# Kernel optimization log

Measured on AMD Instinct MI355X. Metric: run time of the kernel, lower is better.

Reference implementation:

```python
import jax, jax.numpy as jnp
import numpy as np

WINDOW_SIZE = 11
SIGMA = 1.5
K2 = 0.03
PAD = WINDOW_SIZE // 2


def _gaussian_window(size, sigma):
    coords = np.arange(size, dtype=np.float32) - size // 2
    g = np.exp(-coords ** 2 / (2.0 * sigma ** 2))
    g = g / g.sum()
    w2d = np.outer(g, g)  # [size, size]
    return jnp.asarray(w2d[None, None], dtype=jnp.float32)  # [1,1,size,size]


def _blur(x, w):
    # x: [B,1,H,W], w: [1,1,k,k]; SAME zero padding, matches F.conv2d(padding=k//2)
    return jax.lax.conv_general_dilated(
        x, w, window_strides=(1, 1), padding=[(PAD, PAD), (PAD, PAD)],
        dimension_numbers=("NCHW", "OIHW", "NCHW"))


def setup_inputs() -> dict:
    key = jax.random.key(0)
    k1, k2 = jax.random.split(key)
    B, C, H, W = 32, 1, 512, 512
    inp = jax.random.uniform(k1, (B, C, H, W), dtype=jnp.float32)
    tgt = jax.random.uniform(k2, (B, C, H, W), dtype=jnp.float32)
    mask = jnp.ones((B, C, H, W), dtype=jnp.float32)
    window = _gaussian_window(WINDOW_SIZE, SIGMA)
    return {"input": inp, "target": tgt, "mask": mask, "window": window}


def reference(input, target, mask, window):
    # mask application (mask path is always exercised, matching the torch code)
    inp = input * mask
    tgt = target * mask

    mw = _blur(mask, window) + 1e-08  # blurred mask normalizer

    mu_i = _blur(inp, window) / mw
    mu_t = _blur(tgt, window) / mw

    sigma_i_sq = _blur(inp * inp, window) / mw - mu_i * mu_i
    sigma_t_sq = _blur(tgt * tgt, window) / mw - mu_t * mu_t
    sigma_it = _blur(inp * tgt, window) / mw - mu_i * mu_t

    L = jnp.maximum(jnp.max(inp), jnp.max(tgt))
    C2 = (K2 * L) ** 2
    C3 = C2 / 2.0

    sigma_i = jnp.sqrt(jax.nn.relu(sigma_i_sq) + 1e-12)
    sigma_t = jnp.sqrt(jax.nn.relu(sigma_t_sq) + 1e-12)

    structure_map = (sigma_it + C3) / (sigma_i * sigma_t + C3 + 1e-08)
    return 1.0 - jnp.mean(structure_map)
```

## Files before the change

kernel.cpp:

```cpp
#include <hip/hip_runtime.h>
#include <math.h>

#define BATCH 32
#define H 512
#define W 512
#define TX 32
#define TY 32
#define SX 44
#define NPIX (32LL*512*512)

__device__ inline void atomicMaxFloat(float* addr, float val) {
    unsigned int* ua = (unsigned int*)addr;
    unsigned int old = __float_as_uint(*addr);
    while (true) {
        float of = __uint_as_float(old);
        if (of >= val) break;
        unsigned int assumed = old;
        old = atomicCAS(ua, assumed, __float_as_uint(val));
        if (old == assumed) break;
    }
}

__global__ void init_kernel(double* sum, float* mx) {
    *sum = 0.0;
    *mx = -INFINITY;
}

__global__ __launch_bounds__(256) void maxred_kernel(
        const float* __restrict__ in, const float* __restrict__ tg,
        const float* __restrict__ mk, float* mx) {
    const float4* in4 = (const float4*)in;
    const float4* tg4 = (const float4*)tg;
    const float4* mk4 = (const float4*)mk;
    long long n4 = NPIX / 4;
    long long idx = (long long)blockIdx.x * blockDim.x + threadIdx.x;
    long long stride = (long long)gridDim.x * blockDim.x;
    float m = -INFINITY;
    for (long long i = idx; i < n4; i += stride) {
        float4 a = in4[i], b = tg4[i], c = mk4[i];
        m = fmaxf(m, fmaxf(a.x * c.x, b.x * c.x));
        m = fmaxf(m, fmaxf(a.y * c.y, b.y * c.y));
        m = fmaxf(m, fmaxf(a.z * c.z, b.z * c.z));
        m = fmaxf(m, fmaxf(a.w * c.w, b.w * c.w));
    }
    for (int off = 32; off; off >>= 1) m = fmaxf(m, __shfl_down(m, off, 64));
    __shared__ float smax[4];
    int lane = threadIdx.x & 63, wid = threadIdx.x >> 6;
    if (lane == 0) smax[wid] = m;
    __syncthreads();
    if (threadIdx.x == 0) {
        float r = fmaxf(fmaxf(smax[0], smax[1]), fmaxf(smax[2], smax[3]));
        atomicMaxFloat(mx, r);
    }
}

__global__ __launch_bounds__(256, 4) void ssim_kernel(
        const float* __restrict__ in, const float* __restrict__ tg,
        const float* __restrict__ mk, const float* __restrict__ win,
        const float* __restrict__ mxp, double* __restrict__ sum) {
    __shared__ __align__(16) float vch[6][TY][SX];
    __shared__ float gw[11];
    __shared__ float ssum[4];

    int t = threadIdx.x;
    if (t < 11) {
        float s = 0.f;
        #pragma unroll
        for (int j = 0; j < 11; j++) s += win[t * 11 + j];
        gw[t] = s;
    }
    __syncthreads();

    float gr[11];
    #pragma unroll
    for (int k = 0; k < 11; k++) gr[k] = gw[k];

    int img = blockIdx.z;
    int y0 = blockIdx.y * TY, x0 = blockIdx.x * TX;
    const size_t base = (size_t)img * H * W;
    const float* inb = in + base;
    const float* tgb = tg + base;
    const float* mkb = mk + base;

    if (t < 168) {
        int s = t / 42, cc = t - s * 42;
        int x = x0 - 5 + cc;
        bool inx = (unsigned)x < (unsigned)W;
        float acc[6][8];
        #pragma unroll
        for (int ch = 0; ch < 6; ch++)
            #pragma unroll
            for (int u = 0; u < 8; u++) acc[ch][u] = 0.f;

        int ybase = y0 + 8 * s - 5;
        #pragma unroll
        for (int j = 0; j < 18; j++) {
            int y = ybase + j;
            float m = 0.f, iv = 0.f, tv = 0.f;
            if (inx && (unsigned)y < (unsigned)H) {
                size_t g = (size_t)y * W + x;
                m = mkb[g]; iv = inb[g]; tv = tgb[g];
            }
            float a = iv * m, b = tv * m;
            float v[6] = { m, a, b, a * a, b * b, a * b };
            #pragma unroll
            for (int u = 0; u < 8; u++) {
                int k = j - u;
                if (k >= 0 && k < 11) {
                    float w = gr[k];
                    #pragma unroll
                    for (int ch = 0; ch < 6; ch++) acc[ch][u] += w * v[ch];
                }
            }
        }
        #pragma unroll
        for (int u = 0; u < 8; u++) {
            int rr = 8 * s + u;
            #pragma unroll
            for (int ch = 0; ch < 6; ch++) vch[ch][rr][cc + 2] = acc[ch][u];
        }
    }
    __syncthreads();

    float L = *mxp;
    float C3 = 0.5f * (0.03f * L) * (0.03f * L);

    int r = t >> 3, c0 = (t & 7) << 2;
    float hs[6][4];
    #pragma unroll
    for (int ch = 0; ch < 6; ch++) {
        float Wl[16];
        #pragma unroll
        for (int q = 0; q < 4; q++) {
            float4 v = *(const float4*)&vch[ch][r][c0 + 4 * q];
            Wl[4 * q + 0] = v.x; Wl[4 * q + 1] = v.y;
            Wl[4 * q + 2] = v.z; Wl[4 * q + 3] = v.w;
        }
        #pragma unroll
        for (int u = 0; u < 4; u++) {
            float h = 0.f;
            #pragma unroll
            for (int k = 0; k < 11; k++) h += gr[k] * Wl[u + 2 + k];
            hs[ch][u] = h;
        }
    }

    float lsum = 0.f;
    #pragma unroll
    for (int u = 0; u < 4; u++) {
        float mw = hs[0][u] + 1e-8f;
        float inv = 1.0f / mw;
        float mu_i = hs[1][u] * inv, mu_t = hs[2][u] * inv;
        float si2 = hs[3][u] * inv - mu_i * mu_i;
        float st2 = hs[4][u] * inv - mu_t * mu_t;
        float sit = hs[5][u] * inv - mu_i * mu_t;
        float si = sqrtf(fmaxf(si2, 0.f) + 1e-12f);
        float st = sqrtf(fmaxf(st2, 0.f) + 1e-12f);
        lsum += (sit + C3) / (si * st + C3 + 1e-8f);
    }

    for (int off = 32; off; off >>= 1) lsum += __shfl_down(lsum, off, 64);
    int lane = t & 63, wid = t >> 6;
    if (lane == 0) ssum[wid] = lsum;
    __syncthreads();
    if (t == 0) {
        float tot = ssum[0] + ssum[1] + ssum[2] + ssum[3];
        atomicAdd(sum, (double)tot);
    }
}

__global__ void fin_kernel(const double* __restrict__ sum, float* __restrict__ out) {
    out[0] = 1.0f - (float)(*sum / (double)NPIX);
}

extern "C" void kernel_launch(void* const* d_in, const int* in_sizes, int n_in,
                              void* d_out, int out_size, void* d_ws, size_t ws_size,
                              hipStream_t stream) {
    const float* in  = (const float*)d_in[0];
    const float* tg  = (const float*)d_in[1];
    const float* mk  = (const float*)d_in[2];
    const float* win = (const float*)d_in[3];
    float* out = (float*)d_out;

    double* dsum = (double*)d_ws;
    float*  dmax = (float*)((char*)d_ws + 8);

    init_kernel<<<1, 1, 0, stream>>>(dsum, dmax);
    maxred_kernel<<<2048, 256, 0, stream>>>(in, tg, mk, dmax);
    ssim_kernel<<<dim3(16, 16, 32), 256, 0, stream>>>(in, tg, mk, win, dmax, dsum);
    fin_kernel<<<1, 1, 0, stream>>>(dsum, out);
}
```

Measured before the change: 153.8 us.

## Streamline SSIM kernel: branchless loads, uniform weights, fused ratio math, integer atomic max

Several independent micro-optimisations land together. The CAS-loop float max becomes an integer atomicMax on an order-preserving encoding, and the init kernel becomes a memset. The vertical pass gets a fast path with no bounds checks for interior tiles and clamped loads with zero scaling at the edges. The weights are made wave-uniform through readfirstlane, and the final SSIM expression is rewritten to cross-multiply by the mask weight, using one sqrt and a hardware reciprocal instead of two sqrts and divides. The approximate rcp and sqrt builtins and the reordered arithmetic can shift results slightly.

```diff
diff --git a/kernel.cpp b/kernel.cpp
--- a/kernel.cpp
+++ b/kernel.cpp
@@ -1,7 +1,6 @@
 #include <hip/hip_runtime.h>
 #include <math.h>
 
-#define BATCH 32
 #define H 512
 #define W 512
 #define TX 32
@@ -9,40 +8,32 @@
 #define SX 44
 #define NPIX (32LL*512*512)
 
-__device__ inline void atomicMaxFloat(float* addr, float val) {
-    unsigned int* ua = (unsigned int*)addr;
-    unsigned int old = __float_as_uint(*addr);
-    while (true) {
-        float of = __uint_as_float(old);
-        if (of >= val) break;
-        unsigned int assumed = old;
-        old = atomicCAS(ua, assumed, __float_as_uint(val));
-        if (old == assumed) break;
-    }
-}
-
-__global__ void init_kernel(double* sum, float* mx) {
-    *sum = 0.0;
-    *mx = -INFINITY;
+__device__ inline unsigned encf(float f) {
+    unsigned u = __float_as_uint(f);
+    return (u & 0x80000000u) ? ~u : (u | 0x80000000u);
+}
+__device__ inline float decf(unsigned e) {
+    unsigned u = (e & 0x80000000u) ? (e ^ 0x80000000u) : ~e;
+    return __uint_as_float(u);
 }
 
 __global__ __launch_bounds__(256) void maxred_kernel(
         const float* __restrict__ in, const float* __restrict__ tg,
-        const float* __restrict__ mk, float* mx) {
+        const float* __restrict__ mk, unsigned* __restrict__ mx) {
     const float4* in4 = (const float4*)in;
     const float4* tg4 = (const float4*)tg;
     const float4* mk4 = (const float4*)mk;
     long long n4 = NPIX / 4;
     long long idx = (long long)blockIdx.x * blockDim.x + threadIdx.x;
     long long stride = (long long)gridDim.x * blockDim.x;
-    float m = -INFINITY;
+    float ma = -INFINITY, mb = -INFINITY;
     for (long long i = idx; i < n4; i += stride) {
         float4 a = in4[i], b = tg4[i], c = mk4[i];
-        m = fmaxf(m, fmaxf(a.x * c.x, b.x * c.x));
-        m = fmaxf(m, fmaxf(a.y * c.y, b.y * c.y));
-        m = fmaxf(m, fmaxf(a.z * c.z, b.z * c.z));
-        m = fmaxf(m, fmaxf(a.w * c.w, b.w * c.w));
-    }
+        ma = fmaxf(ma, fmaxf(fmaxf(a.x * c.x, a.y * c.y), fmaxf(a.z * c.z, a.w * c.w)));
+        mb = fmaxf(mb, fmaxf(fmaxf(b.x * c.x, b.y * c.y), fmaxf(b.z * c.z, b.w * c.w)));
+    }
+    float m = fmaxf(ma, mb);
+    #pragma unroll
     for (int off = 32; off; off >>= 1) m = fmaxf(m, __shfl_down(m, off, 64));
     __shared__ float smax[4];
     int lane = threadIdx.x & 63, wid = threadIdx.x >> 6;
@@ -50,14 +41,14 @@
     __syncthreads();
     if (threadIdx.x == 0) {
         float r = fmaxf(fmaxf(smax[0], smax[1]), fmaxf(smax[2], smax[3]));
-        atomicMaxFloat(mx, r);
+        atomicMax(mx, encf(r));
     }
 }
 
 __global__ __launch_bounds__(256, 4) void ssim_kernel(
         const float* __restrict__ in, const float* __restrict__ tg,
         const float* __restrict__ mk, const float* __restrict__ win,
-        const float* __restrict__ mxp, double* __restrict__ sum) {
+        const unsigned* __restrict__ mxp, double* __restrict__ sum) {
     __shared__ __align__(16) float vch[6][TY][SX];
     __shared__ float gw[11];
     __shared__ float ssum[4];
@@ -69,11 +60,14 @@
         for (int j = 0; j < 11; j++) s += win[t * 11 + j];
         gw[t] = s;
     }
-    __syncthreads();
-
-    float gr[11];
-    #pragma unroll
-    for (int k = 0; k < 11; k++) gr[k] = gw[k];
+    float L = decf(*mxp);
+    float C3 = 0.5f * (0.03f * L) * (0.03f * L);
+    __syncthreads();
+
+    float wk[11];
+    #pragma unroll
+    for (int k = 0; k < 11; k++)
+        wk[k] = __uint_as_float(__builtin_amdgcn_readfirstlane(__float_as_uint(gw[k])));
 
     int img = blockIdx.z;
     int y0 = blockIdx.y * TY, x0 = blockIdx.x * TX;
@@ -86,44 +80,64 @@
         int s = t / 42, cc = t - s * 42;
         int x = x0 - 5 + cc;
         bool inx = (unsigned)x < (unsigned)W;
+        int xc = inx ? x : 0;
+        float xs = inx ? 1.f : 0.f;
+        int ybase = y0 + 8 * s - 5;
         float acc[6][8];
         #pragma unroll
         for (int ch = 0; ch < 6; ch++)
             #pragma unroll
             for (int u = 0; u < 8; u++) acc[ch][u] = 0.f;
 
-        int ybase = y0 + 8 * s - 5;
-        #pragma unroll
-        for (int j = 0; j < 18; j++) {
-            int y = ybase + j;
-            float m = 0.f, iv = 0.f, tv = 0.f;
-            if (inx && (unsigned)y < (unsigned)H) {
-                size_t g = (size_t)y * W + x;
-                m = mkb[g]; iv = inb[g]; tv = tgb[g];
-            }
-            float a = iv * m, b = tv * m;
-            float v[6] = { m, a, b, a * a, b * b, a * b };
-            #pragma unroll
-            for (int u = 0; u < 8; u++) {
-                int k = j - u;
-                if (k >= 0 && k < 11) {
-                    float w = gr[k];
-                    #pragma unroll
-                    for (int ch = 0; ch < 6; ch++) acc[ch][u] += w * v[ch];
+        if (ybase >= 0 && ybase <= H - 18) {
+            size_t g = (size_t)ybase * W + xc;
+            #pragma unroll
+            for (int j = 0; j < 18; j++) {
+                float m = mkb[g], iv = inb[g], tv = tgb[g];
+                g += W;
+                float a = iv * m, b = tv * m;
+                float v[6] = { m, a, b, a * a, b * b, a * b };
+                #pragma unroll
+                for (int u = 0; u < 8; u++) {
+                    int k = j - u;
+                    if (k >= 0 && k < 11) {
+                        float w = wk[k];
+                        #pragma unroll
+                        for (int ch = 0; ch < 6; ch++)
+                            acc[ch][u] = fmaf(w, v[ch], acc[ch][u]);
+                    }
                 }
             }
+        } else {
+            #pragma unroll
+            for (int j = 0; j < 18; j++) {
+                int y = ybase + j;
+                bool yok = (unsigned)y < (unsigned)H;
+                size_t g = (size_t)(yok ? y : 0) * W + xc;
+                float sc = yok ? 1.f : 0.f;
+                float m = mkb[g] * sc, iv = inb[g] * sc, tv = tgb[g] * sc;
+                float a = iv * m, b = tv * m;
+                float v[6] = { m, a, b, a * a, b * b, a * b };
+                #pragma unroll
+                for (int u = 0; u < 8; u++) {
+                    int k = j - u;
+                    if (k >= 0 && k < 11) {
+                        float w = wk[k];
+                        #pragma unroll
+                        for (int ch = 0; ch < 6; ch++)
+                            acc[ch][u] = fmaf(w, v[ch], acc[ch][u]);
+                    }
+                }
+            }
         }
         #pragma unroll
         for (int u = 0; u < 8; u++) {
             int rr = 8 * s + u;
             #pragma unroll
-            for (int ch = 0; ch < 6; ch++) vch[ch][rr][cc + 2] = acc[ch][u];
-        }
-    }
-    __syncthreads();
-
-    float L = *mxp;
-    float C3 = 0.5f * (0.03f * L) * (0.03f * L);
+            for (int ch = 0; ch < 6; ch++) vch[ch][rr][cc + 2] = acc[ch][u] * xs;
+        }
+    }
+    __syncthreads();
 
     int r = t >> 3, c0 = (t & 7) << 2;
     float hs[6][4];
@@ -140,7 +154,7 @@
         for (int u = 0; u < 4; u++) {
             float h = 0.f;
             #pragma unroll
-            for (int k = 0; k < 11; k++) h += gr[k] * Wl[u + 2 + k];
+            for (int k = 0; k < 11; k++) h = fmaf(wk[k], Wl[u + 2 + k], h);
             hs[ch][u] = h;
         }
     }
@@ -148,17 +162,18 @@
     float lsum = 0.f;
     #pragma unroll
     for (int u = 0; u < 4; u++) {
+        float h1 = hs[1][u], h2 = hs[2][u];
         float mw = hs[0][u] + 1e-8f;
-        float inv = 1.0f / mw;
-        float mu_i = hs[1][u] * inv, mu_t = hs[2][u] * inv;
-        float si2 = hs[3][u] * inv - mu_i * mu_i;
-        float st2 = hs[4][u] * inv - mu_t * mu_t;
-        float sit = hs[5][u] * inv - mu_i * mu_t;
-        float si = sqrtf(fmaxf(si2, 0.f) + 1e-12f);
-        float st = sqrtf(fmaxf(st2, 0.f) + 1e-12f);
-        lsum += (sit + C3) / (si * st + C3 + 1e-8f);
-    }
-
+        float mw2 = mw * mw;
+        float e12 = 1e-12f * mw2;
+        float Xi = fmaxf(fmaf(hs[3][u], mw, -h1 * h1), 0.f) + e12;
+        float Xt = fmaxf(fmaf(hs[4][u], mw, -h2 * h2), 0.f) + e12;
+        float num = fmaf(hs[5][u], mw, -h1 * h2) + C3 * mw2;
+        float den = __builtin_amdgcn_sqrtf(Xi * Xt) + (C3 + 1e-8f) * mw2;
+        lsum += num * __builtin_amdgcn_rcpf(den);
+    }
+
+    #pragma unroll
     for (int off = 32; off; off >>= 1) lsum += __shfl_down(lsum, off, 64);
     int lane = t & 63, wid = t >> 6;
     if (lane == 0) ssum[wid] = lsum;
@@ -182,10 +197,10 @@
     const float* win = (const float*)d_in[3];
     float* out = (float*)d_out;
 
-    double* dsum = (double*)d_ws;
-    float*  dmax = (float*)((char*)d_ws + 8);
-
-    init_kernel<<<1, 1, 0, stream>>>(dsum, dmax);
+    double*   dsum = (double*)d_ws;
+    unsigned* dmax = (unsigned*)((char*)d_ws + 8);
+
+    hipMemsetAsync(d_ws, 0, 12, stream);
     maxred_kernel<<<2048, 256, 0, stream>>>(in, tg, mk, dmax);
     ssim_kernel<<<dim3(16, 16, 32), 256, 0, stream>>>(in, tg, mk, win, dmax, dsum);
     fin_kernel<<<1, 1, 0, stream>>>(dsum, out);
```

Result: slower. 158.2 us (+2.8%).
